# Performance work log

Hardware: AMD Instinct MI355X
Metric: run time of the kernel (lower is better)

The kernel has to match this reference:

```python
import jax, jax.numpy as jnp
import numpy as np

N_NODES = 50000
N_EDGES = 800000
IN_DIM, HID_DIM, OUT_DIM = 128, 128, 64


def setup_inputs() -> dict:
    key = jax.random.key(0)
    ks = jax.random.split(key, 12)
    x = jax.random.normal(ks[0], (N_NODES, IN_DIM), dtype=jnp.float32)
    src = jax.random.randint(ks[1], (N_EDGES,), 0, N_NODES, dtype=jnp.int32)
    dst = jax.random.randint(ks[2], (N_EDGES,), 0, N_NODES, dtype=jnp.int32)
    def lin(k, fan_in, fan_out):
        s = 1.0 / np.sqrt(fan_in)
        kw, kb = jax.random.split(k)
        W = jax.random.uniform(kw, (fan_in, fan_out), jnp.float32, -s, s)
        b = jax.random.uniform(kb, (fan_out,), jnp.float32, -s, s)
        return W, b
    W1, b1 = lin(ks[3], IN_DIM, HID_DIM)
    W2, b2 = lin(ks[4], HID_DIM, HID_DIM)
    W3, b3 = lin(ks[5], HID_DIM, OUT_DIM)
    Wf, bf = lin(ks[6], OUT_DIM, 1)
    return {"x": x, "src": src, "dst": dst,
            "W1": W1, "b1": b1, "W2": W2, "b2": b2,
            "W3": W3, "b3": b3, "Wf": Wf, "bf": bf}


def reference(x, src, dst, W1, b1, W2, b2, W3, b3, Wf, bf):
    n = x.shape[0]
    # GCN symmetric norm with self-loops: deg = in-degree + 1 (self loop)
    ones = jnp.ones(src.shape[0], x.dtype)
    deg = jax.ops.segment_sum(ones, dst, num_segments=n) + 1.0
    dinv = jax.lax.rsqrt(deg)                       # [N]
    edge_norm = dinv[src] * dinv[dst]               # [E]
    self_norm = dinv * dinv                         # [N], self-loop weight

    def gcn(h, W, b):
        h = h @ W                                   # transform first (PyG order)
        agg = jax.ops.segment_sum(h[src] * edge_norm[:, None], dst, num_segments=n)
        agg = agg + h * self_norm[:, None]          # self-loop contribution
        return agg + b

    h = jax.nn.relu(gcn(x, W1, b1))
    h = jax.nn.relu(gcn(h, W2, b2))
    h = jax.nn.relu(gcn(h, W3, b3))
    return h @ Wf + bf                              # [N, 1] per-node scores
```

## Files before the change

### kernel.cpp

```cpp
#include <hip/hip_runtime.h>
#include <hip/hip_bf16.h>

typedef short bf16x8 __attribute__((ext_vector_type(8)));
typedef float f32x4 __attribute__((ext_vector_type(4)));
typedef _Float16 f16x2 __attribute__((ext_vector_type(2)));
typedef unsigned short u16x8 __attribute__((ext_vector_type(8)));

static __device__ __forceinline__ unsigned short f2bf_rne(float f) {
    unsigned int u = __float_as_uint(f);
    u += 0x7fff + ((u >> 16) & 1);
    return (unsigned short)(u >> 16);
}
static __device__ __forceinline__ float bf2f(unsigned short h) {
    return __uint_as_float(((unsigned int)h) << 16);
}

static __device__ __forceinline__ void wsplit_one(const float* W, unsigned short* hi,
                                                  unsigned short* lo, int BN, int idx) {
    int k = idx / BN, n = idx % BN;
    float w = W[idx];
    unsigned short h = f2bf_rne(w);
    unsigned short l = f2bf_rne(w - bf2f(h));
    int CT = BN >> 4;
    int kc = k >> 5, quad = (k >> 3) & 3, j = k & 7;
    int ct = n >> 4, c = n & 15;
    int slot = (((kc * CT + ct) * 4 + quad) * 16 + c) * 8 + j;
    hi[slot] = h;
    lo[slot] = l;
}


template<int BN>
static __device__ __forceinline__ void gemm_body_f32(const float* __restrict__ A,
                        const unsigned short* __restrict__ Whi, const unsigned short* __restrict__ Wlo,
                        _Float16* __restrict__ C, int N, int blk,
                        unsigned short* AhiS, unsigned short* AloS) {
    constexpr int CT = BN / 16;
    const int tid = threadIdx.x;
    const int wave = tid >> 6;
    const int lane = tid & 63;
    const int quad = lane >> 4;
    const int c16 = lane & 15;
    const int row0 = blk * 64;

    f32x4 acc[CT];
    #pragma unroll
    for (int t = 0; t < CT; ++t) acc[t] = (f32x4){0.f, 0.f, 0.f, 0.f};

    for (int kc = 0; kc < 4; ++kc) {
        #pragma unroll
        for (int r = 0; r < 2; ++r) {
            int f4 = tid + r * 256;
            int arow = f4 >> 3;
            int c4 = f4 & 7;
            int grow = row0 + arow;
            float4 v = make_float4(0.f, 0.f, 0.f, 0.f);
            if (grow < N) v = *(const float4*)&A[(size_t)grow * 128 + kc * 32 + c4 * 4];
            unsigned short h0 = f2bf_rne(v.x), h1 = f2bf_rne(v.y), h2 = f2bf_rne(v.z), h3 = f2bf_rne(v.w);
            ushort4 hv = make_ushort4(h0, h1, h2, h3);
            ushort4 lv = make_ushort4(f2bf_rne(v.x - bf2f(h0)), f2bf_rne(v.y - bf2f(h1)),
                                      f2bf_rne(v.z - bf2f(h2)), f2bf_rne(v.w - bf2f(h3)));
            int q = c4 >> 1;
            int joff = (c4 & 1) * 4;
            int base = (q * 64 + arow) * 8 + joff;
            *(ushort4*)&AhiS[base] = hv;
            *(ushort4*)&AloS[base] = lv;
        }
        __syncthreads();

        int abase = (quad * 64 + wave * 16 + c16) * 8;
        bf16x8 ahi = *(const bf16x8*)&AhiS[abase];
        bf16x8 alo = *(const bf16x8*)&AloS[abase];

        #pragma unroll
        for (int ct = 0; ct < CT; ++ct) {
            size_t bslot = ((size_t)(kc * CT + ct) * 64 + lane) * 8;
            bf16x8 bhi = *(const bf16x8*)&Whi[bslot];
            bf16x8 blo = *(const bf16x8*)&Wlo[bslot];
            acc[ct] = __builtin_amdgcn_mfma_f32_16x16x32_bf16(ahi, bhi, acc[ct], 0, 0, 0);
            acc[ct] = __builtin_amdgcn_mfma_f32_16x16x32_bf16(ahi, blo, acc[ct], 0, 0, 0);
            acc[ct] = __builtin_amdgcn_mfma_f32_16x16x32_bf16(alo, bhi, acc[ct], 0, 0, 0);
        }
        __syncthreads();
    }

    #pragma unroll
    for (int ct = 0; ct < CT; ++ct) {
        #pragma unroll
        for (int r = 0; r < 4; ++r) {
            int grow = row0 + wave * 16 + quad * 4 + r;
            if (grow < N) C[(size_t)grow * BN + ct * 16 + c16] = (_Float16)acc[ct][r];
        }
    }
}

template<int BN>
static __device__ __forceinline__ void gemm_body_bf(const unsigned short* __restrict__ Ahi,
                        const unsigned short* __restrict__ Alo,
                        const unsigned short* __restrict__ Whi, const unsigned short* __restrict__ Wlo,
                        _Float16* __restrict__ C, int N, int blk,
                        unsigned short* AhiS, unsigned short* AloS) {
    constexpr int CT = BN / 16;
    const int tid = threadIdx.x;
    const int wave = tid >> 6;
    const int lane = tid & 63;
    const int quad = lane >> 4;
    const int c16 = lane & 15;
    const int row0 = blk * 64;
    const int arow = tid >> 2;
    const int cblk = tid & 3;
    const int grow = row0 + arow;
    const bool inb = grow < N;
    const size_t agbase = (size_t)grow * 128 + cblk * 8;
    const int sbase = (cblk * 64 + arow) * 8;

    f32x4 acc[CT];
    #pragma unroll
    for (int t = 0; t < CT; ++t) acc[t] = (f32x4){0.f, 0.f, 0.f, 0.f};

    for (int kc = 0; kc < 4; ++kc) {
        u16x8 hv = {0, 0, 0, 0, 0, 0, 0, 0};
        u16x8 lv = {0, 0, 0, 0, 0, 0, 0, 0};
        if (inb) {
            hv = *(const u16x8*)&Ahi[agbase + kc * 32];
            lv = *(const u16x8*)&Alo[agbase + kc * 32];
        }
        *(u16x8*)&AhiS[sbase] = hv;
        *(u16x8*)&AloS[sbase] = lv;
        __syncthreads();

        int abase = (quad * 64 + wave * 16 + c16) * 8;
        bf16x8 ahi = *(const bf16x8*)&AhiS[abase];
        bf16x8 alo = *(const bf16x8*)&AloS[abase];

        #pragma unroll
        for (int ct = 0; ct < CT; ++ct) {
            size_t bslot = ((size_t)(kc * CT + ct) * 64 + lane) * 8;
            bf16x8 bhi = *(const bf16x8*)&Whi[bslot];
            bf16x8 blo = *(const bf16x8*)&Wlo[bslot];
            acc[ct] = __builtin_amdgcn_mfma_f32_16x16x32_bf16(ahi, bhi, acc[ct], 0, 0, 0);
            acc[ct] = __builtin_amdgcn_mfma_f32_16x16x32_bf16(ahi, blo, acc[ct], 0, 0, 0);
            acc[ct] = __builtin_amdgcn_mfma_f32_16x16x32_bf16(alo, bhi, acc[ct], 0, 0, 0);
        }
        __syncthreads();
    }

    #pragma unroll
    for (int ct = 0; ct < CT; ++ct) {
        #pragma unroll
        for (int r = 0; r < 4; ++r) {
            int gr = row0 + wave * 16 + quad * 4 + r;
            if (gr < N) C[(size_t)gr * BN + ct * 16 + c16] = (_Float16)acc[ct][r];
        }
    }
}


__global__ __launch_bounds__(256) void k_count_wsplit(const int* __restrict__ dst, int* __restrict__ deg,
                          int* __restrict__ rank,
                          const float* __restrict__ W1, const float* __restrict__ W2, const float* __restrict__ W3,
                          unsigned short* __restrict__ W1hi, unsigned short* __restrict__ W1lo,
                          unsigned short* __restrict__ W2hi, unsigned short* __restrict__ W2lo,
                          unsigned short* __restrict__ W3hi, unsigned short* __restrict__ W3lo,
                          int E) {
    int e = blockIdx.x * blockDim.x + threadIdx.x;
    if (e < E) rank[e] = atomicAdd(&deg[dst[e]], 1);
    if (e < 128 * 128) {
        wsplit_one(W1, W1hi, W1lo, 128, e);
        wsplit_one(W2, W2hi, W2lo, 128, e);
    }
    if (e < 128 * 64) wsplit_one(W3, W3hi, W3lo, 64, e);
}

__global__ __launch_bounds__(1024) void k_scan(const int* __restrict__ deg, float* __restrict__ dinv,
                                               int* __restrict__ row_start, int N) {
    __shared__ int s[1024];
    __shared__ int wsum[16];
    __shared__ int prefix;
    const int t = threadIdx.x;
    const int base = blockIdx.x * 1024;

    {
        int v = 0;
        for (int j = t; j < base; j += 1024) v += deg[j];
        for (int off = 32; off > 0; off >>= 1) v += __shfl_down(v, off, 64);
        if ((t & 63) == 0) wsum[t >> 6] = v;
        __syncthreads();
        if (t == 0) {
            int acc = 0;
            #pragma unroll
            for (int k = 0; k < 16; ++k) acc += wsum[k];
            prefix = acc;
        }
    }

    int i = base + t;
    int v = 0;
    if (i < N) {
        v = deg[i];
        dinv[i] = rsqrtf((float)v + 1.0f);
    }
    s[t] = v;
    __syncthreads();
    for (int off = 1; off < 1024; off <<= 1) {
        int x = (t >= off) ? s[t - off] : 0;
        __syncthreads();
        s[t] += x;
        __syncthreads();
    }
    if (i <= N) row_start[i] = prefix + s[t] - v;
}


__global__ __launch_bounds__(256, 2) void k_gemm1_scatter(const float* __restrict__ A,
                          const unsigned short* __restrict__ Whi, const unsigned short* __restrict__ Wlo,
                          _Float16* __restrict__ C, int N, int gemmGrid,
                          const int* __restrict__ src, const int* __restrict__ dst,
                          const int* __restrict__ row_start, const int* __restrict__ rank,
                          const float* __restrict__ dinv, int2* __restrict__ cv, int E) {
    __shared__ unsigned short AhiS[4 * 64 * 8];
    __shared__ unsigned short AloS[4 * 64 * 8];
    if ((int)blockIdx.x < gemmGrid) {
        gemm_body_f32<128>(A, Whi, Wlo, C, N, blockIdx.x, AhiS, AloS);
    } else {
        int e = (blockIdx.x - gemmGrid) * 256 + threadIdx.x;
        if (e < E) {
            int d = dst[e];
            int s = src[e];
            cv[row_start[d] + rank[e]] = make_int2(s, __float_as_int(dinv[s]));
        }
    }
}

template<int BN>
__global__ __launch_bounds__(256, 2) void k_gemm_bf(const unsigned short* __restrict__ Ahi,
                        const unsigned short* __restrict__ Alo,
                        const unsigned short* __restrict__ Whi, const unsigned short* __restrict__ Wlo,
                        _Float16* __restrict__ C, int N) {
    __shared__ unsigned short AhiS[4 * 64 * 8];
    __shared__ unsigned short AloS[4 * 64 * 8];
    gemm_body_bf<BN>(Ahi, Alo, Whi, Wlo, C, N, blockIdx.x, AhiS, AloS);
}


__global__ __launch_bounds__(256) void k_agg128(const _Float16* __restrict__ t,
                      unsigned short* __restrict__ outHi, unsigned short* __restrict__ outLo,
                      const int* __restrict__ row_start, const int2* __restrict__ cv,
                      const float* __restrict__ dinv, const float* __restrict__ bias,
                      int N) {
    int gid = blockIdx.x * blockDim.x + threadIdx.x;
    int node = gid >> 6;
    int lane = gid & 63;
    if (node >= N) return;
    int p = row_start[node];
    int end = row_start[node + 1];
    const f16x2* tp = (const f16x2*)t;
    float2 acc[4];
    #pragma unroll
    for (int j = 0; j < 4; ++j) acc[j] = make_float2(0.f, 0.f);

    while (p < end) {
        int idx = p + lane;
        int2 h = (idx < end) ? cv[idx] : make_int2(0, 0);
        int cnt = min(end - p, 64);
        int rounds = (cnt + 15) >> 4;
        for (int r = 0; r < rounds; ++r) {
            int base = r * 16;
            int s[16]; float w[16];
            #pragma unroll
            for (int j = 0; j < 16; ++j) {
                s[j] = __builtin_amdgcn_readlane(h.x, base + j);
                w[j] = __int_as_float(__builtin_amdgcn_readlane(h.y, base + j));
            }
            f16x2 v[16];
            #pragma unroll
            for (int j = 0; j < 16; ++j) v[j] = tp[s[j] * 64 + lane];
            #pragma unroll
            for (int j = 0; j < 16; ++j) {
                acc[j & 3].x += w[j] * (float)v[j].x;
                acc[j & 3].y += w[j] * (float)v[j].y;
            }
        }
        p += 64;
    }
    float di = dinv[node];
    f16x2 sv = tp[node * 64 + lane];
    float2 bv = ((const float2*)bias)[lane];
    float sx = (acc[0].x + acc[1].x) + (acc[2].x + acc[3].x);
    float sy = (acc[0].y + acc[1].y) + (acc[2].y + acc[3].y);
    float rx = fmaxf(di * sx + di * di * (float)sv.x + bv.x, 0.f);
    float ry = fmaxf(di * sy + di * di * (float)sv.y + bv.y, 0.f);
    unsigned short hx = f2bf_rne(rx), hy = f2bf_rne(ry);
    unsigned short lx = f2bf_rne(rx - bf2f(hx)), ly = f2bf_rne(ry - bf2f(hy));
    ushort2 hw; hw.x = hx; hw.y = hy;
    ushort2 lw; lw.x = lx; lw.y = ly;
    ((ushort2*)outHi)[(size_t)node * 64 + lane] = hw;
    ((ushort2*)outLo)[(size_t)node * 64 + lane] = lw;
}

__global__ __launch_bounds__(256) void k_agg64_final(const _Float16* __restrict__ t, float* __restrict__ outp,
                      const int* __restrict__ row_start, const int2* __restrict__ cv,
                      const float* __restrict__ dinv, const float* __restrict__ bias,
                      const float* __restrict__ Wf, const float* __restrict__ bf,
                      int N) {
    int gid = blockIdx.x * blockDim.x + threadIdx.x;
    int node = gid >> 6;
    int lane = gid & 63;
    if (node >= N) return;
    int p = row_start[node];
    int end = row_start[node + 1];
    float acc[4] = {0.f, 0.f, 0.f, 0.f};

    while (p < end) {
        int idx = p + lane;
        int2 h = (idx < end) ? cv[idx] : make_int2(0, 0);
        int cnt = min(end - p, 64);
        int rounds = (cnt + 15) >> 4;
        for (int r = 0; r < rounds; ++r) {
            int base = r * 16;
            int s[16]; float w[16];
            #pragma unroll
            for (int j = 0; j < 16; ++j) {
                s[j] = __builtin_amdgcn_readlane(h.x, base + j);
                w[j] = __int_as_float(__builtin_amdgcn_readlane(h.y, base + j));
            }
            _Float16 v[16];
            #pragma unroll
            for (int j = 0; j < 16; ++j) v[j] = t[s[j] * 64 + lane];
            #pragma unroll
            for (int j = 0; j < 16; ++j) acc[j & 3] += w[j] * (float)v[j];
        }
        p += 64;
    }
    float di = dinv[node];
    float r = di * ((acc[0] + acc[1]) + (acc[2] + acc[3])) + di * di * (float)t[node * 64 + lane] + bias[lane];
    r = fmaxf(r, 0.f);
    float v = r * Wf[lane];
    for (int off = 32; off > 0; off >>= 1) v += __shfl_down(v, off, 64);
    if (lane == 0) outp[node] = v + bf[0];
}


extern "C" void kernel_launch(void* const* d_in, const int* in_sizes, int n_in,
                              void* d_out, int out_size, void* d_ws, size_t ws_size,
                              hipStream_t stream) {
    const float* x  = (const float*)d_in[0];
    const int*   src = (const int*)d_in[1];
    const int*   dst = (const int*)d_in[2];
    const float* W1 = (const float*)d_in[3];
    const float* b1 = (const float*)d_in[4];
    const float* W2 = (const float*)d_in[5];
    const float* b2 = (const float*)d_in[6];
    const float* W3 = (const float*)d_in[7];
    const float* b3 = (const float*)d_in[8];
    const float* Wf = (const float*)d_in[9];
    const float* bf = (const float*)d_in[10];
    float* out = (float*)d_out;

    const int N = 50000;
    const int E = 800000;

    char* ws = (char*)d_ws;
    size_t off = 0;
    auto alloc = [&](size_t bytes) -> void* {
        void* p = (void*)(ws + off);
        off += (bytes + 511) & ~((size_t)511);
        return p;
    };
    int*   deg       = (int*)alloc((size_t)N * 4);
    float* dinv      = (float*)alloc((size_t)N * 4);
    int*   row_start = (int*)alloc((size_t)(N + 1) * 4);
    int*   rank      = (int*)alloc((size_t)E * 4);
    int2*  cv        = (int2*)alloc((size_t)E * 8);
    _Float16* bufT   = (_Float16*)alloc((size_t)N * 128 * 2);
    unsigned short* bufHi = (unsigned short*)alloc((size_t)N * 128 * 2);
    unsigned short* bufLo = (unsigned short*)alloc((size_t)N * 128 * 2);
    unsigned short* W1hi = (unsigned short*)alloc(128 * 128 * 2);
    unsigned short* W1lo = (unsigned short*)alloc(128 * 128 * 2);
    unsigned short* W2hi = (unsigned short*)alloc(128 * 128 * 2);
    unsigned short* W2lo = (unsigned short*)alloc(128 * 128 * 2);
    unsigned short* W3hi = (unsigned short*)alloc(128 * 64 * 2);
    unsigned short* W3lo = (unsigned short*)alloc(128 * 64 * 2);

    hipMemsetAsync(deg, 0, (size_t)N * 4, stream);

    k_count_wsplit<<<(E + 255) / 256, 256, 0, stream>>>(dst, deg, rank, W1, W2, W3,
                                                        W1hi, W1lo, W2hi, W2lo, W3hi, W3lo, E);
    int NB = (N + 1023) / 1024;
    k_scan<<<NB, 1024, 0, stream>>>(deg, dinv, row_start, N);

    int gemmGrid = (N + 63) / 64;
    int scatGrid = (E + 255) / 256;
    int aggGrid = (N * 64 + 255) / 256;

    k_gemm1_scatter<<<gemmGrid + scatGrid, 256, 0, stream>>>(x, W1hi, W1lo, bufT, N, gemmGrid,
                                                             src, dst, row_start, rank, dinv, cv, E);
    k_agg128<<<aggGrid, 256, 0, stream>>>(bufT, bufHi, bufLo, row_start, cv, dinv, b1, N);
    k_gemm_bf<128><<<gemmGrid, 256, 0, stream>>>(bufHi, bufLo, W2hi, W2lo, bufT, N);
    k_agg128<<<aggGrid, 256, 0, stream>>>(bufT, bufHi, bufLo, row_start, cv, dinv, b2, N);
    k_gemm_bf<64><<<gemmGrid, 256, 0, stream>>>(bufHi, bufLo, W3hi, W3lo, bufT, N);
    k_agg64_final<<<aggGrid, 256, 0, stream>>>(bufT, out, row_start, cv, dinv, b3, Wf, bf, N);
}
```

Before: 273.4 us.

## Gather neighbor rows with 16-byte vector loads across lane groups in aggregation

New measurement: 275.1 us. About the same (+0.6%).

```diff
diff --git a/kernel.cpp b/kernel.cpp
--- a/kernel.cpp
+++ b/kernel.cpp
@@ -4,6 +4,7 @@
 typedef short bf16x8 __attribute__((ext_vector_type(8)));
 typedef float f32x4 __attribute__((ext_vector_type(4)));
 typedef _Float16 f16x2 __attribute__((ext_vector_type(2)));
+typedef _Float16 f16x8v __attribute__((ext_vector_type(8)));
 typedef unsigned short u16x8 __attribute__((ext_vector_type(8)));
 
 static __device__ __forceinline__ unsigned short f2bf_rne(float f) {
@@ -252,50 +253,51 @@
     int node = gid >> 6;
     int lane = gid & 63;
     if (node >= N) return;
+    int l16 = lane & 15;
+    int g4 = lane >> 4;
     int p = row_start[node];
     int end = row_start[node + 1];
-    const f16x2* tp = (const f16x2*)t;
-    float2 acc[4];
-    #pragma unroll
-    for (int j = 0; j < 4; ++j) acc[j] = make_float2(0.f, 0.f);
+    const f16x8v* tp8 = (const f16x8v*)t;
+    float a[8];
+    #pragma unroll
+    for (int d = 0; d < 8; ++d) a[d] = 0.f;
 
     while (p < end) {
-        int idx = p + lane;
+        int idx = p + l16;
         int2 h = (idx < end) ? cv[idx] : make_int2(0, 0);
-        int cnt = min(end - p, 64);
-        int rounds = (cnt + 15) >> 4;
-        for (int r = 0; r < rounds; ++r) {
-            int base = r * 16;
-            int s[16]; float w[16];
+        #pragma unroll
+        for (int jj = 0; jj < 4; ++jj) {
+            int sl = jj * 4 + g4;
+            int s = __shfl(h.x, sl, 64);
+            float w = __int_as_float(__shfl(h.y, sl, 64));
+            f16x8v v = tp8[(size_t)s * 16 + l16];
             #pragma unroll
-            for (int j = 0; j < 16; ++j) {
-                s[j] = __builtin_amdgcn_readlane(h.x, base + j);
-                w[j] = __int_as_float(__builtin_amdgcn_readlane(h.y, base + j));
-            }
-            f16x2 v[16];
-            #pragma unroll
-            for (int j = 0; j < 16; ++j) v[j] = tp[s[j] * 64 + lane];
-            #pragma unroll
-            for (int j = 0; j < 16; ++j) {
-                acc[j & 3].x += w[j] * (float)v[j].x;
-                acc[j & 3].y += w[j] * (float)v[j].y;
-            }
-        }
-        p += 64;
+            for (int d = 0; d < 8; ++d) a[d] += w * (float)v[d];
+        }
+        p += 16;
+    }
+    #pragma unroll
+    for (int d = 0; d < 8; ++d) {
+        a[d] += __shfl_xor(a[d], 16, 64);
+        a[d] += __shfl_xor(a[d], 32, 64);
     }
     float di = dinv[node];
-    f16x2 sv = tp[node * 64 + lane];
-    float2 bv = ((const float2*)bias)[lane];
-    float sx = (acc[0].x + acc[1].x) + (acc[2].x + acc[3].x);
-    float sy = (acc[0].y + acc[1].y) + (acc[2].y + acc[3].y);
-    float rx = fmaxf(di * sx + di * di * (float)sv.x + bv.x, 0.f);
-    float ry = fmaxf(di * sy + di * di * (float)sv.y + bv.y, 0.f);
-    unsigned short hx = f2bf_rne(rx), hy = f2bf_rne(ry);
-    unsigned short lx = f2bf_rne(rx - bf2f(hx)), ly = f2bf_rne(ry - bf2f(hy));
-    ushort2 hw; hw.x = hx; hw.y = hy;
-    ushort2 lw; lw.x = lx; lw.y = ly;
-    ((ushort2*)outHi)[(size_t)node * 64 + lane] = hw;
-    ((ushort2*)outLo)[(size_t)node * 64 + lane] = lw;
+    f16x8v sv = tp8[(size_t)node * 16 + l16];
+    float4 b0 = ((const float4*)bias)[l16 * 2];
+    float4 b1 = ((const float4*)bias)[l16 * 2 + 1];
+    float bb[8] = {b0.x, b0.y, b0.z, b0.w, b1.x, b1.y, b1.z, b1.w};
+    u16x8 hw, lw;
+    #pragma unroll
+    for (int d = 0; d < 8; ++d) {
+        float r = fmaxf(di * a[d] + di * di * (float)sv[d] + bb[d], 0.f);
+        unsigned short hx = f2bf_rne(r);
+        hw[d] = hx;
+        lw[d] = f2bf_rne(r - bf2f(hx));
+    }
+    if (g4 == 0) {
+        *(u16x8*)&outHi[(size_t)node * 128 + l16 * 8] = hw;
+        *(u16x8*)&outLo[(size_t)node * 128 + l16 * 8] = lw;
+    }
 }
 
 __global__ __launch_bounds__(256) void k_agg64_final(const _Float16* __restrict__ t, float* __restrict__ outp,
@@ -307,37 +309,53 @@
     int node = gid >> 6;
     int lane = gid & 63;
     if (node >= N) return;
+    int l8 = lane & 7;
+    int g8 = lane >> 3;
     int p = row_start[node];
     int end = row_start[node + 1];
-    float acc[4] = {0.f, 0.f, 0.f, 0.f};
+    const f16x8v* tp8 = (const f16x8v*)t;
+    float a[8];
+    #pragma unroll
+    for (int d = 0; d < 8; ++d) a[d] = 0.f;
 
     while (p < end) {
-        int idx = p + lane;
+        int idx = p + (lane & 15);
         int2 h = (idx < end) ? cv[idx] : make_int2(0, 0);
-        int cnt = min(end - p, 64);
-        int rounds = (cnt + 15) >> 4;
-        for (int r = 0; r < rounds; ++r) {
-            int base = r * 16;
-            int s[16]; float w[16];
+        #pragma unroll
+        for (int jj = 0; jj < 2; ++jj) {
+            int sl = jj * 8 + g8;
+            int s = __shfl(h.x, sl, 64);
+            float w = __int_as_float(__shfl(h.y, sl, 64));
+            f16x8v v = tp8[(size_t)s * 8 + l8];
             #pragma unroll
-            for (int j = 0; j < 16; ++j) {
-                s[j] = __builtin_amdgcn_readlane(h.x, base + j);
-                w[j] = __int_as_float(__builtin_amdgcn_readlane(h.y, base + j));
-            }
-            _Float16 v[16];
-            #pragma unroll
-            for (int j = 0; j < 16; ++j) v[j] = t[s[j] * 64 + lane];
-            #pragma unroll
-            for (int j = 0; j < 16; ++j) acc[j & 3] += w[j] * (float)v[j];
-        }
-        p += 64;
+            for (int d = 0; d < 8; ++d) a[d] += w * (float)v[d];
+        }
+        p += 16;
+    }
+    #pragma unroll
+    for (int d = 0; d < 8; ++d) {
+        a[d] += __shfl_xor(a[d], 8, 64);
+        a[d] += __shfl_xor(a[d], 16, 64);
+        a[d] += __shfl_xor(a[d], 32, 64);
     }
     float di = dinv[node];
-    float r = di * ((acc[0] + acc[1]) + (acc[2] + acc[3])) + di * di * (float)t[node * 64 + lane] + bias[lane];
-    r = fmaxf(r, 0.f);
-    float v = r * Wf[lane];
-    for (int off = 32; off > 0; off >>= 1) v += __shfl_down(v, off, 64);
-    if (lane == 0) outp[node] = v + bf[0];
+    f16x8v sv = tp8[(size_t)node * 8 + l8];
+    float4 b0 = ((const float4*)bias)[l8 * 2];
+    float4 b1 = ((const float4*)bias)[l8 * 2 + 1];
+    float bb[8] = {b0.x, b0.y, b0.z, b0.w, b1.x, b1.y, b1.z, b1.w};
+    float4 w0 = ((const float4*)Wf)[l8 * 2];
+    float4 w1 = ((const float4*)Wf)[l8 * 2 + 1];
+    float ww[8] = {w0.x, w0.y, w0.z, w0.w, w1.x, w1.y, w1.z, w1.w};
+    float dot = 0.f;
+    #pragma unroll
+    for (int d = 0; d < 8; ++d) {
+        float r = fmaxf(di * a[d] + di * di * (float)sv[d] + bb[d], 0.f);
+        dot += r * ww[d];
+    }
+    dot += __shfl_xor(dot, 1, 64);
+    dot += __shfl_xor(dot, 2, 64);
+    dot += __shfl_xor(dot, 4, 64);
+    if (lane == 0) outp[node] = dot + bf[0];
 }
 
 
```

## Fuse layer aggregation into following GEMM via shared-memory staged activations

Applied to the files above, without the earlier changes.

Result: slower. 291.5 us (+6.6%).

```diff
diff --git a/kernel.cpp b/kernel.cpp
--- a/kernel.cpp
+++ b/kernel.cpp
@@ -4,7 +4,6 @@
 typedef short bf16x8 __attribute__((ext_vector_type(8)));
 typedef float f32x4 __attribute__((ext_vector_type(4)));
 typedef _Float16 f16x2 __attribute__((ext_vector_type(2)));
-typedef unsigned short u16x8 __attribute__((ext_vector_type(8)));
 
 static __device__ __forceinline__ unsigned short f2bf_rne(float f) {
     unsigned int u = __float_as_uint(f);
@@ -94,67 +93,6 @@
     }
 }
 
-template<int BN>
-static __device__ __forceinline__ void gemm_body_bf(const unsigned short* __restrict__ Ahi,
-                        const unsigned short* __restrict__ Alo,
-                        const unsigned short* __restrict__ Whi, const unsigned short* __restrict__ Wlo,
-                        _Float16* __restrict__ C, int N, int blk,
-                        unsigned short* AhiS, unsigned short* AloS) {
-    constexpr int CT = BN / 16;
-    const int tid = threadIdx.x;
-    const int wave = tid >> 6;
-    const int lane = tid & 63;
-    const int quad = lane >> 4;
-    const int c16 = lane & 15;
-    const int row0 = blk * 64;
-    const int arow = tid >> 2;
-    const int cblk = tid & 3;
-    const int grow = row0 + arow;
-    const bool inb = grow < N;
-    const size_t agbase = (size_t)grow * 128 + cblk * 8;
-    const int sbase = (cblk * 64 + arow) * 8;
-
-    f32x4 acc[CT];
-    #pragma unroll
-    for (int t = 0; t < CT; ++t) acc[t] = (f32x4){0.f, 0.f, 0.f, 0.f};
-
-    for (int kc = 0; kc < 4; ++kc) {
-        u16x8 hv = {0, 0, 0, 0, 0, 0, 0, 0};
-        u16x8 lv = {0, 0, 0, 0, 0, 0, 0, 0};
-        if (inb) {
-            hv = *(const u16x8*)&Ahi[agbase + kc * 32];
-            lv = *(const u16x8*)&Alo[agbase + kc * 32];
-        }
-        *(u16x8*)&AhiS[sbase] = hv;
-        *(u16x8*)&AloS[sbase] = lv;
-        __syncthreads();
-
-        int abase = (quad * 64 + wave * 16 + c16) * 8;
-        bf16x8 ahi = *(const bf16x8*)&AhiS[abase];
-        bf16x8 alo = *(const bf16x8*)&AloS[abase];
-
-        #pragma unroll
-        for (int ct = 0; ct < CT; ++ct) {
-            size_t bslot = ((size_t)(kc * CT + ct) * 64 + lane) * 8;
-            bf16x8 bhi = *(const bf16x8*)&Whi[bslot];
-            bf16x8 blo = *(const bf16x8*)&Wlo[bslot];
-            acc[ct] = __builtin_amdgcn_mfma_f32_16x16x32_bf16(ahi, bhi, acc[ct], 0, 0, 0);
-            acc[ct] = __builtin_amdgcn_mfma_f32_16x16x32_bf16(ahi, blo, acc[ct], 0, 0, 0);
-            acc[ct] = __builtin_amdgcn_mfma_f32_16x16x32_bf16(alo, bhi, acc[ct], 0, 0, 0);
-        }
-        __syncthreads();
-    }
-
-    #pragma unroll
-    for (int ct = 0; ct < CT; ++ct) {
-        #pragma unroll
-        for (int r = 0; r < 4; ++r) {
-            int gr = row0 + wave * 16 + quad * 4 + r;
-            if (gr < N) C[(size_t)gr * BN + ct * 16 + c16] = (_Float16)acc[ct][r];
-        }
-    }
-}
-
 
 __global__ __launch_bounds__(256) void k_count_wsplit(const int* __restrict__ dst, int* __restrict__ deg,
                           int* __restrict__ rank,
@@ -232,71 +170,107 @@
     }
 }
 
+
 template<int BN>
-__global__ __launch_bounds__(256, 2) void k_gemm_bf(const unsigned short* __restrict__ Ahi,
-                        const unsigned short* __restrict__ Alo,
+__global__ __launch_bounds__(256, 2) void k_fused_agg_gemm(const _Float16* __restrict__ t,
                         const unsigned short* __restrict__ Whi, const unsigned short* __restrict__ Wlo,
-                        _Float16* __restrict__ C, int N) {
-    __shared__ unsigned short AhiS[4 * 64 * 8];
-    __shared__ unsigned short AloS[4 * 64 * 8];
-    gemm_body_bf<BN>(Ahi, Alo, Whi, Wlo, C, N, blockIdx.x, AhiS, AloS);
-}
-
-
-__global__ __launch_bounds__(256) void k_agg128(const _Float16* __restrict__ t,
-                      unsigned short* __restrict__ outHi, unsigned short* __restrict__ outLo,
-                      const int* __restrict__ row_start, const int2* __restrict__ cv,
-                      const float* __restrict__ dinv, const float* __restrict__ bias,
-                      int N) {
-    int gid = blockIdx.x * blockDim.x + threadIdx.x;
-    int node = gid >> 6;
-    int lane = gid & 63;
-    if (node >= N) return;
-    int p = row_start[node];
-    int end = row_start[node + 1];
+                        _Float16* __restrict__ C,
+                        const int* __restrict__ row_start, const int2* __restrict__ cv,
+                        const float* __restrict__ dinv, const float* __restrict__ bias,
+                        int N) {
+    constexpr int CT = BN / 16;
+    __shared__ unsigned short AhiS[16 * 64 * 8];
+    __shared__ unsigned short AloS[16 * 64 * 8];
+    const int tid = threadIdx.x;
+    const int wave = tid >> 6;
+    const int lane = tid & 63;
+    const int row0 = blockIdx.x * 64;
     const f16x2* tp = (const f16x2*)t;
-    float2 acc[4];
-    #pragma unroll
-    for (int j = 0; j < 4; ++j) acc[j] = make_float2(0.f, 0.f);
-
-    while (p < end) {
-        int idx = p + lane;
-        int2 h = (idx < end) ? cv[idx] : make_int2(0, 0);
-        int cnt = min(end - p, 64);
-        int rounds = (cnt + 15) >> 4;
-        for (int r = 0; r < rounds; ++r) {
-            int base = r * 16;
-            int s[16]; float w[16];
-            #pragma unroll
-            for (int j = 0; j < 16; ++j) {
-                s[j] = __builtin_amdgcn_readlane(h.x, base + j);
-                w[j] = __int_as_float(__builtin_amdgcn_readlane(h.y, base + j));
+    const float2 bv = ((const float2*)bias)[lane];
+    const int d2 = lane * 2;
+    const int lslot = (((d2 >> 5) * 4 + ((d2 >> 3) & 3)) * 64) * 8 + (d2 & 7);
+
+    for (int i = 0; i < 16; ++i) {
+        const int arow = wave * 16 + i;
+        const int node = row0 + arow;
+        float rx = 0.f, ry = 0.f;
+        if (node < N) {
+            int p = row_start[node];
+            int end = row_start[node + 1];
+            float2 acc[4];
+            #pragma unroll
+            for (int j = 0; j < 4; ++j) acc[j] = make_float2(0.f, 0.f);
+            while (p < end) {
+                int idx = p + lane;
+                int2 h = (idx < end) ? cv[idx] : make_int2(0, 0);
+                int cnt = min(end - p, 64);
+                int rounds = (cnt + 15) >> 4;
+                for (int r = 0; r < rounds; ++r) {
+                    int base = r * 16;
+                    int s[16]; float w[16];
+                    #pragma unroll
+                    for (int j = 0; j < 16; ++j) {
+                        s[j] = __builtin_amdgcn_readlane(h.x, base + j);
+                        w[j] = __int_as_float(__builtin_amdgcn_readlane(h.y, base + j));
+                    }
+                    f16x2 v[16];
+                    #pragma unroll
+                    for (int j = 0; j < 16; ++j) v[j] = tp[s[j] * 64 + lane];
+                    #pragma unroll
+                    for (int j = 0; j < 16; ++j) {
+                        acc[j & 3].x += w[j] * (float)v[j].x;
+                        acc[j & 3].y += w[j] * (float)v[j].y;
+                    }
+                }
+                p += 64;
             }
-            f16x2 v[16];
-            #pragma unroll
-            for (int j = 0; j < 16; ++j) v[j] = tp[s[j] * 64 + lane];
-            #pragma unroll
-            for (int j = 0; j < 16; ++j) {
-                acc[j & 3].x += w[j] * (float)v[j].x;
-                acc[j & 3].y += w[j] * (float)v[j].y;
-            }
-        }
-        p += 64;
-    }
-    float di = dinv[node];
-    f16x2 sv = tp[node * 64 + lane];
-    float2 bv = ((const float2*)bias)[lane];
-    float sx = (acc[0].x + acc[1].x) + (acc[2].x + acc[3].x);
-    float sy = (acc[0].y + acc[1].y) + (acc[2].y + acc[3].y);
-    float rx = fmaxf(di * sx + di * di * (float)sv.x + bv.x, 0.f);
-    float ry = fmaxf(di * sy + di * di * (float)sv.y + bv.y, 0.f);
-    unsigned short hx = f2bf_rne(rx), hy = f2bf_rne(ry);
-    unsigned short lx = f2bf_rne(rx - bf2f(hx)), ly = f2bf_rne(ry - bf2f(hy));
-    ushort2 hw; hw.x = hx; hw.y = hy;
-    ushort2 lw; lw.x = lx; lw.y = ly;
-    ((ushort2*)outHi)[(size_t)node * 64 + lane] = hw;
-    ((ushort2*)outLo)[(size_t)node * 64 + lane] = lw;
-}
+            float di = dinv[node];
+            f16x2 sv = tp[node * 64 + lane];
+            float sx = (acc[0].x + acc[1].x) + (acc[2].x + acc[3].x);
+            float sy = (acc[0].y + acc[1].y) + (acc[2].y + acc[3].y);
+            rx = fmaxf(di * sx + di * di * (float)sv.x + bv.x, 0.f);
+            ry = fmaxf(di * sy + di * di * (float)sv.y + bv.y, 0.f);
+        }
+        unsigned short hx = f2bf_rne(rx), hy = f2bf_rne(ry);
+        unsigned short lx = f2bf_rne(rx - bf2f(hx)), ly = f2bf_rne(ry - bf2f(hy));
+        ushort2 hw; hw.x = hx; hw.y = hy;
+        ushort2 lw; lw.x = lx; lw.y = ly;
+        int b = lslot + arow * 8;
+        *(ushort2*)&AhiS[b] = hw;
+        *(ushort2*)&AloS[b] = lw;
+    }
+    __syncthreads();
+
+    const int quad = lane >> 4;
+    const int c16 = lane & 15;
+    f32x4 acc[CT];
+    #pragma unroll
+    for (int ct = 0; ct < CT; ++ct) acc[ct] = (f32x4){0.f, 0.f, 0.f, 0.f};
+    #pragma unroll
+    for (int kc = 0; kc < 4; ++kc) {
+        int abase = ((kc * 4 + quad) * 64 + wave * 16 + c16) * 8;
+        bf16x8 ahi = *(const bf16x8*)&AhiS[abase];
+        bf16x8 alo = *(const bf16x8*)&AloS[abase];
+        #pragma unroll
+        for (int ct = 0; ct < CT; ++ct) {
+            size_t bslot = ((size_t)(kc * CT + ct) * 64 + lane) * 8;
+            bf16x8 bhi = *(const bf16x8*)&Whi[bslot];
+            bf16x8 blo = *(const bf16x8*)&Wlo[bslot];
+            acc[ct] = __builtin_amdgcn_mfma_f32_16x16x32_bf16(ahi, bhi, acc[ct], 0, 0, 0);
+            acc[ct] = __builtin_amdgcn_mfma_f32_16x16x32_bf16(ahi, blo, acc[ct], 0, 0, 0);
+            acc[ct] = __builtin_amdgcn_mfma_f32_16x16x32_bf16(alo, bhi, acc[ct], 0, 0, 0);
+        }
+    }
+    #pragma unroll
+    for (int ct = 0; ct < CT; ++ct) {
+        #pragma unroll
+        for (int r = 0; r < 4; ++r) {
+            int gr = row0 + wave * 16 + quad * 4 + r;
+            if (gr < N) C[(size_t)gr * BN + ct * 16 + c16] = (_Float16)acc[ct][r];
+        }
+    }
+}
+
 
 __global__ __launch_bounds__(256) void k_agg64_final(const _Float16* __restrict__ t, float* __restrict__ outp,
                       const int* __restrict__ row_start, const int2* __restrict__ cv,
@@ -372,9 +346,8 @@
     int*   row_start = (int*)alloc((size_t)(N + 1) * 4);
     int*   rank      = (int*)alloc((size_t)E * 4);
     int2*  cv        = (int2*)alloc((size_t)E * 8);
-    _Float16* bufT   = (_Float16*)alloc((size_t)N * 128 * 2);
-    unsigned short* bufHi = (unsigned short*)alloc((size_t)N * 128 * 2);
-    unsigned short* bufLo = (unsigned short*)alloc((size_t)N * 128 * 2);
+    _Float16* bufT1  = (_Float16*)alloc((size_t)N * 128 * 2);
+    _Float16* bufT2  = (_Float16*)alloc((size_t)N * 128 * 2);
     unsigned short* W1hi = (unsigned short*)alloc(128 * 128 * 2);
     unsigned short* W1lo = (unsigned short*)alloc(128 * 128 * 2);
     unsigned short* W2hi = (unsigned short*)alloc(128 * 128 * 2);
@@ -393,11 +366,11 @@
     int scatGrid = (E + 255) / 256;
     int aggGrid = (N * 64 + 255) / 256;
 
-    k_gemm1_scatter<<<gemmGrid + scatGrid, 256, 0, stream>>>(x, W1hi, W1lo, bufT, N, gemmGrid,
+    k_gemm1_scatter<<<gemmGrid + scatGrid, 256, 0, stream>>>(x, W1hi, W1lo, bufT1, N, gemmGrid,
                                                              src, dst, row_start, rank, dinv, cv, E);
-    k_agg128<<<aggGrid, 256, 0, stream>>>(bufT, bufHi, bufLo, row_start, cv, dinv, b1, N);
-    k_gemm_bf<128><<<gemmGrid, 256, 0, stream>>>(bufHi, bufLo, W2hi, W2lo, bufT, N);
-    k_agg128<<<aggGrid, 256, 0, stream>>>(bufT, bufHi, bufLo, row_start, cv, dinv, b2, N);
-    k_gemm_bf<64><<<gemmGrid, 256, 0, stream>>>(bufHi, bufLo, W3hi, W3lo, bufT, N);
-    k_agg64_final<<<aggGrid, 256, 0, stream>>>(bufT, out, row_start, cv, dinv, b3, Wf, bf, N);
-}
+    k_fused_agg_gemm<128><<<gemmGrid, 256, 0, stream>>>(bufT1, W2hi, W2lo, bufT2,
+                                                        row_start, cv, dinv, b1, N);
+    k_fused_agg_gemm<64><<<gemmGrid, 256, 0, stream>>>(bufT2, W3hi, W3lo, bufT1,
+                                                       row_start, cv, dinv, b2, N);
+    k_agg64_final<<<aggGrid, 256, 0, stream>>>(bufT1, out, row_start, cv, dinv, b3, Wf, bf, N);
+}
```
